# Optimization experiments

Hardware: AMD Instinct MI355X
Metric: run time of the kernel (lower is better)

## Reference

```python
import jax, jax.numpy as jnp
import numpy as np

N = 100000      # nodes
E = 1600000     # edges (avg degree 16)
F_IN = 300      # input feature dim
H = 64          # hidden channels
OUT = 20        # output classes
L = 8           # num GCN2Conv layers
ALPHA = 0.1
THETA = 0.5


def setup_inputs() -> dict:
    key = jax.random.key(0)
    ks = jax.random.split(key, 6)
    x = jax.random.normal(ks[0], (N, F_IN), jnp.float32)
    edge_index = jax.random.randint(ks[1], (2, E), 0, N, dtype=jnp.int32)
    edge_weights = jax.random.uniform(ks[2], (E,), jnp.float32)
    W_in = jax.random.normal(ks[3], (F_IN, H), jnp.float32) / np.sqrt(F_IN)
    b_in = jnp.zeros((H,), jnp.float32)
    conv_w = jax.random.normal(ks[4], (L, H, H), jnp.float32) / np.sqrt(H)
    W_out = jax.random.normal(ks[5], (H, OUT), jnp.float32) / np.sqrt(H)
    b_out = jnp.zeros((OUT,), jnp.float32)
    return dict(x=x, edge_index=edge_index, edge_weights=edge_weights,
                W_in=W_in, b_in=b_in, conv_w=conv_w, W_out=W_out, b_out=b_out)


def _gcn_norm(edge_index, edge_weights, n, dtype):
    # add self-loops with weight 1, symmetric normalization (PyG gcn_norm)
    loop = jnp.arange(n, dtype=edge_index.dtype)
    row = jnp.concatenate([edge_index[0], loop])
    col = jnp.concatenate([edge_index[1], loop])
    w = jnp.concatenate([edge_weights, jnp.ones((n,), dtype)])
    deg = jax.ops.segment_sum(w, col, num_segments=n)
    dinv = jnp.where(deg > 0, jax.lax.rsqrt(deg), 0.0).astype(dtype)
    norm = dinv[row] * w * dinv[col]
    return row, col, norm


def reference(x, edge_index, edge_weights, W_in, b_in, conv_w, W_out, b_out):
    n = x.shape[0]
    row, col, norm = _gcn_norm(edge_index, edge_weights, n, x.dtype)
    # eval mode: dropout is identity
    h = jax.nn.relu(x @ W_in + b_in)   # start_with_lin (F_IN != H)
    x0 = h
    num_layers = conv_w.shape[0]
    for l in range(num_layers):
        beta = float(np.log(THETA / (l + 1) + 1.0))
        # A_hat @ h : gather sources, weight by norm, scatter-add to targets
        agg = jax.ops.segment_sum(norm[:, None] * h[row], col, num_segments=n)
        z = (1.0 - ALPHA) * agg + ALPHA * x0  # initial-residual mixing
        h = jax.nn.relu((1.0 - beta) * z + beta * (z @ conv_w[l]))
    return h @ W_out + b_out
```

## Files before the change

### kernel.cpp

```cpp
#include <hip/hip_runtime.h>
#include <hip/hip_fp16.h>
#include <math.h>


#define HID 64
#define FIN 300
#define NOUT 20
#define ALPHA 0.1f
#define DSCALE 262144.0f
#define CNT_SHIFT 25
#define DEG_MASK 0x1FFFFFFu

typedef _Float16 f16;
typedef f16 f16x8 __attribute__((ext_vector_type(8)));
typedef float f32x4 __attribute__((ext_vector_type(4)));

__device__ __forceinline__ float wdec(unsigned v) {
    union { unsigned short u; __half h; } c;
    c.u = (unsigned short)(v >> 17);
    return __half2float(c.h);
}

__device__ __forceinline__ void unpack8(const float4& v, float* f) {
    const __half2* p = reinterpret_cast<const __half2*>(&v);
#pragma unroll
    for (int i = 0; i < 4; ++i) {
        float2 t = __half22float2(p[i]);
        f[2 * i] = t.x;
        f[2 * i + 1] = t.y;
    }
}

__global__ void init_k(unsigned* __restrict__ packed, int n) {
    int i = blockIdx.x * blockDim.x + threadIdx.x;
    if (i < n) packed[i] = 0u;
}

__global__ void accum_k(const int* __restrict__ col, const float* __restrict__ w,
                        unsigned* __restrict__ packed,
                        unsigned char* __restrict__ rank, int e) {
    int i = blockIdx.x * blockDim.x + threadIdx.x;
    if (i < e) {
        unsigned q = (unsigned)__float2uint_rn(w[i] * DSCALE);
        unsigned old = atomicAdd(&packed[col[i]], (1u << CNT_SHIFT) | q);
        rank[i] = (unsigned char)(old >> CNT_SHIFT);
    }
}

__global__ __launch_bounds__(1024) void unpackscan_k(const unsigned* __restrict__ packed,
                                                     float* __restrict__ dinv,
                                                     int* __restrict__ bsum, int n) {
    __shared__ int s[1024];
    int t = threadIdx.x, i = blockIdx.x * 1024 + t;
    int cnt = 0;
    if (i < n) {
        unsigned v = packed[i];
        cnt = (int)(v >> CNT_SHIFT);
        float d = 1.0f + (float)(v & DEG_MASK) * (1.0f / DSCALE);
        dinv[i] = rsqrtf(d);
    }
    s[t] = cnt;
    __syncthreads();
    for (int off = 512; off > 0; off >>= 1) {
        if (t < off) s[t] += s[t + off];
        __syncthreads();
    }
    if (t == 0) bsum[blockIdx.x] = s[0];
}

__global__ void scan2_k(int* __restrict__ bsum, int nb, int* __restrict__ rp,
                        int n, int e) {
    if (blockIdx.x == 0 && threadIdx.x == 0) {
        int acc = 0;
        for (int b = 0; b < nb; ++b) { int v = bsum[b]; bsum[b] = acc; acc += v; }
        rp[n] = e;
    }
}

__global__ __launch_bounds__(1024) void scan3_k(const unsigned* __restrict__ packed,
                                                const int* __restrict__ bsum,
                                                int* __restrict__ rp, int n) {
    __shared__ int s[1024];
    int t = threadIdx.x, i = blockIdx.x * 1024 + t;
    int v = (i < n) ? (int)(packed[i] >> CNT_SHIFT) : 0;
    s[t] = v;
    __syncthreads();
    for (int off = 1; off < 1024; off <<= 1) {
        int u = (t >= off) ? s[t - off] : 0;
        __syncthreads();
        s[t] += u;
        __syncthreads();
    }
    if (i < n) rp[i] = bsum[blockIdx.x] + s[t] - v;
}

__global__ __launch_bounds__(256) void fill_k(const int* __restrict__ row,
                                              const int* __restrict__ col,
                                              const float* __restrict__ ew,
                                              const float* __restrict__ dinv,
                                              const int* __restrict__ rp,
                                              const unsigned char* __restrict__ rank,
                                              unsigned* __restrict__ edges,
                                              int e, int n) {
    int xcd = blockIdx.x & 7;
    int lo = (int)(((long long)n * xcd) >> 3);
    int hi = (int)(((long long)n * (xcd + 1)) >> 3);
    int nblk = gridDim.x >> 3;
    int stride = nblk * 256;
    for (int i = (blockIdx.x >> 3) * 256 + threadIdx.x; i < e; i += stride) {
        int c = col[i];
        if (c < lo || c >= hi) continue;
        int r = row[i];
        float nw = (1.0f - ALPHA) * dinv[r] * ew[i] * dinv[c];
        union { __half h; unsigned short u; } cv;
        cv.h = __float2half(nw);
        int pos = rp[c] + (int)rank[i];
        edges[pos] = ((unsigned)cv.u << 17) | (unsigned)r;
    }
}

__global__ void wt_k(const float* __restrict__ Win, f16* __restrict__ Wt) {
    int i = blockIdx.x * blockDim.x + threadIdx.x;
    if (i < 64 * 320) {
        int c = i / 320, k = i - c * 320;
        Wt[i] = (k < FIN) ? (f16)Win[k * 64 + c] : (f16)0.0f;
    }
}

__global__ __launch_bounds__(256) void gemm_in_k(const float* __restrict__ x,
                                                 const f16* __restrict__ Wt,
                                                 const float* __restrict__ bin,
                                                 __half* __restrict__ x0h, int n) {
    __shared__ f16 As[64 * 72];
    int t = threadIdx.x, lane = t & 63, wv = t >> 6;
    int node0 = blockIdx.x * 64;
    int lr = lane & 15, kg = lane >> 4;
    f32x4 acc0 = {0, 0, 0, 0}, acc1 = {0, 0, 0, 0}, acc2 = {0, 0, 0, 0}, acc3 = {0, 0, 0, 0};
    int fi = t & 15;
    for (int c = 0; c < 5; ++c) {
        __syncthreads();
#pragma unroll
        for (int it = 0; it < 4; ++it) {
            int row = (t >> 4) + it * 16;
            int rr = node0 + row;
            rr = (rr < n) ? rr : (n - 1);
            int kbase = c * 64 + fi * 4;
            float4 v = make_float4(0.f, 0.f, 0.f, 0.f);
            if (kbase < FIN)
                v = *reinterpret_cast<const float4*>(x + (size_t)rr * FIN + kbase);
            union { float2 f2; f16 h[4]; } u;
            u.h[0] = (f16)v.x; u.h[1] = (f16)v.y; u.h[2] = (f16)v.z; u.h[3] = (f16)v.w;
            *reinterpret_cast<float2*>(As + row * 72 + fi * 4) = u.f2;
        }
        __syncthreads();
#pragma unroll
        for (int ks = 0; ks < 2; ++ks) {
            f16x8 a = *(const f16x8*)(As + (wv * 16 + lr) * 72 + ks * 32 + kg * 8);
            const f16* wb = Wt + c * 64 + ks * 32 + kg * 8;
            f16x8 b0 = *(const f16x8*)(wb + (0 * 16 + lr) * 320);
            f16x8 b1 = *(const f16x8*)(wb + (1 * 16 + lr) * 320);
            f16x8 b2 = *(const f16x8*)(wb + (2 * 16 + lr) * 320);
            f16x8 b3 = *(const f16x8*)(wb + (3 * 16 + lr) * 320);
            acc0 = __builtin_amdgcn_mfma_f32_16x16x32_f16(a, b0, acc0, 0, 0, 0);
            acc1 = __builtin_amdgcn_mfma_f32_16x16x32_f16(a, b1, acc1, 0, 0, 0);
            acc2 = __builtin_amdgcn_mfma_f32_16x16x32_f16(a, b2, acc2, 0, 0, 0);
            acc3 = __builtin_amdgcn_mfma_f32_16x16x32_f16(a, b3, acc3, 0, 0, 0);
        }
    }
    float bi0 = bin[0 * 16 + lr], bi1 = bin[1 * 16 + lr];
    float bi2 = bin[2 * 16 + lr], bi3 = bin[3 * 16 + lr];
    f16 ov[4][4];
#pragma unroll
    for (int r = 0; r < 4; ++r) {
        ov[0][r] = (f16)fmaxf(acc0[r] + bi0, 0.f);
        ov[1][r] = (f16)fmaxf(acc1[r] + bi1, 0.f);
        ov[2][r] = (f16)fmaxf(acc2[r] + bi2, 0.f);
        ov[3][r] = (f16)fmaxf(acc3[r] + bi3, 0.f);
    }
    __syncthreads();
#pragma unroll
    for (int cg = 0; cg < 4; ++cg)
#pragma unroll
        for (int r = 0; r < 4; ++r)
            As[(wv * 16 + kg * 4 + r) * 72 + cg * 16 + lr] = ov[cg][r];
    __syncthreads();
#pragma unroll
    for (int it = 0; it < 2; ++it) {
        int idx = t + it * 256;
        int row = idx >> 3, ch = idx & 7;
        int node = node0 + row;
        if (node < n)
            ((float4*)(x0h + (size_t)node * 64))[ch] =
                *reinterpret_cast<const float4*>(As + row * 72 + ch * 8);
    }
}

__global__ __launch_bounds__(256) void layer_k(const int* __restrict__ rp,
                                               const unsigned* __restrict__ edges,
                                               const float* __restrict__ dinv,
                                               const __half* __restrict__ x0h,
                                               const __half* __restrict__ hin,
                                               __half* __restrict__ hout,
                                               const float* __restrict__ Wl,
                                               float beta, int n) {
    __shared__ f16 As[64 * 72];
    __shared__ f16 Bs[64 * 72];
    int t = threadIdx.x, lane = t & 63, wv = t >> 6;
    int node0 = blockIdx.x * 64;
    for (int i = t; i < 4096; i += 256) {
        int k = i >> 6, c = i & 63;
        Bs[c * 72 + k] = (f16)Wl[i];
    }
    int g = lane >> 3, c8 = lane & 7;
#pragma unroll
    for (int pass = 0; pass < 2; ++pass) {
        int row = pass * 32 + wv * 8 + g;
        int node = node0 + row;
        int nd = (node < n) ? node : (n - 1);
        int j = rp[nd], end = (node < n) ? rp[nd + 1] : j;
        float a0[8], a1[8];
#pragma unroll
        for (int i = 0; i < 8; ++i) { a0[i] = 0.f; a1[i] = 0.f; }
        while (__any(j < end)) {
            bool v0 = j < end, v1 = (j + 1) < end;
            unsigned e0 = edges[v0 ? j : 0];
            unsigned e1 = edges[v1 ? (j + 1) : 0];
            float w0 = v0 ? wdec(e0) : 0.f;
            float w1 = v1 ? wdec(e1) : 0.f;
            float4 r0 = ((const float4*)(hin + (size_t)(e0 & 0x1FFFF) * 64))[c8];
            float4 r1 = ((const float4*)(hin + (size_t)(e1 & 0x1FFFF) * 64))[c8];
            float f0[8], f1[8];
            unpack8(r0, f0);
            unpack8(r1, f1);
#pragma unroll
            for (int i = 0; i < 8; ++i) {
                a0[i] = fmaf(w0, f0[i], a0[i]);
                a1[i] = fmaf(w1, f1[i], a1[i]);
            }
            j += 2;
        }
        float di = dinv[nd];
        float c1 = (1.0f - ALPHA) * di * di;
        float4 hs4 = ((const float4*)(hin + (size_t)nd * 64))[c8];
        float4 xs4 = ((const float4*)(x0h + (size_t)nd * 64))[c8];
        float hf[8], xf[8];
        unpack8(hs4, hf);
        unpack8(xs4, xf);
        f16x8 zv8;
#pragma unroll
        for (int i = 0; i < 8; ++i)
            zv8[i] = (f16)fmaf(ALPHA, xf[i], fmaf(c1, hf[i], a0[i] + a1[i]));
        *(f16x8*)(As + row * 72 + c8 * 8) = zv8;
    }
    __syncthreads();
    int lr = lane & 15, kg = lane >> 4;
    f32x4 acc0 = {0, 0, 0, 0}, acc1 = {0, 0, 0, 0}, acc2 = {0, 0, 0, 0}, acc3 = {0, 0, 0, 0};
    f16x8 af0 = *(const f16x8*)(As + (wv * 16 + lr) * 72 + kg * 8);
    f16x8 af1 = *(const f16x8*)(As + (wv * 16 + lr) * 72 + 32 + kg * 8);
    {
        f16x8 b0 = *(const f16x8*)(Bs + (0 * 16 + lr) * 72 + kg * 8);
        f16x8 b1 = *(const f16x8*)(Bs + (0 * 16 + lr) * 72 + 32 + kg * 8);
        acc0 = __builtin_amdgcn_mfma_f32_16x16x32_f16(af0, b0, acc0, 0, 0, 0);
        acc0 = __builtin_amdgcn_mfma_f32_16x16x32_f16(af1, b1, acc0, 0, 0, 0);
    }
    {
        f16x8 b0 = *(const f16x8*)(Bs + (1 * 16 + lr) * 72 + kg * 8);
        f16x8 b1 = *(const f16x8*)(Bs + (1 * 16 + lr) * 72 + 32 + kg * 8);
        acc1 = __builtin_amdgcn_mfma_f32_16x16x32_f16(af0, b0, acc1, 0, 0, 0);
        acc1 = __builtin_amdgcn_mfma_f32_16x16x32_f16(af1, b1, acc1, 0, 0, 0);
    }
    {
        f16x8 b0 = *(const f16x8*)(Bs + (2 * 16 + lr) * 72 + kg * 8);
        f16x8 b1 = *(const f16x8*)(Bs + (2 * 16 + lr) * 72 + 32 + kg * 8);
        acc2 = __builtin_amdgcn_mfma_f32_16x16x32_f16(af0, b0, acc2, 0, 0, 0);
        acc2 = __builtin_amdgcn_mfma_f32_16x16x32_f16(af1, b1, acc2, 0, 0, 0);
    }
    {
        f16x8 b0 = *(const f16x8*)(Bs + (3 * 16 + lr) * 72 + kg * 8);
        f16x8 b1 = *(const f16x8*)(Bs + (3 * 16 + lr) * 72 + 32 + kg * 8);
        acc3 = __builtin_amdgcn_mfma_f32_16x16x32_f16(af0, b0, acc3, 0, 0, 0);
        acc3 = __builtin_amdgcn_mfma_f32_16x16x32_f16(af1, b1, acc3, 0, 0, 0);
    }
    float omb = 1.0f - beta;
    f16 ov[4][4];
#pragma unroll
    for (int cg = 0; cg < 4; ++cg) {
        f32x4 acc = (cg == 0) ? acc0 : (cg == 1) ? acc1 : (cg == 2) ? acc2 : acc3;
        int col = cg * 16 + lr;
#pragma unroll
        for (int r = 0; r < 4; ++r) {
            float zv = (float)As[(wv * 16 + kg * 4 + r) * 72 + col];
            ov[cg][r] = (f16)fmaxf(fmaf(beta, acc[r], omb * zv), 0.f);
        }
    }
    __syncthreads();
#pragma unroll
    for (int cg = 0; cg < 4; ++cg)
#pragma unroll
        for (int r = 0; r < 4; ++r)
            As[(wv * 16 + kg * 4 + r) * 72 + cg * 16 + lr] = ov[cg][r];
    __syncthreads();
#pragma unroll
    for (int it = 0; it < 2; ++it) {
        int idx = t + it * 256;
        int row = idx >> 3, ch = idx & 7;
        int node = node0 + row;
        if (node < n)
            ((float4*)(hout + (size_t)node * 64))[ch] =
                *reinterpret_cast<const float4*>(As + row * 72 + ch * 8);
    }
}

__global__ __launch_bounds__(256) void gemm_out_k(const __half* __restrict__ h,
                                                  const float* __restrict__ Wout,
                                                  const float* __restrict__ bout,
                                                  float* __restrict__ out, int n) {
    __shared__ float hs[64][65];
    __shared__ float Ws[64 * NOUT];
    __shared__ float bs[NOUT];
    int t = threadIdx.x;
    for (int i = t; i < 64 * NOUT; i += 256) Ws[i] = Wout[i];
    if (t < NOUT) bs[t] = bout[t];
    int base = blockIdx.x * 64;
    int lim = min(64, n - base);
    for (int i = t; i < 64 * 32; i += 256) {
        int r = i >> 5, c2 = (i & 31) * 2;
        float2 v = make_float2(0.f, 0.f);
        if (r < lim) {
            __half2 hv = reinterpret_cast<const __half2*>(
                h + (size_t)(base + r) * 64)[i & 31];
            v = __half22float2(hv);
        }
        hs[r][c2] = v.x;
        hs[r][c2 + 1] = v.y;
    }
    __syncthreads();
#pragma unroll
    for (int q = 0; q < 5; ++q) {
        int of = t + 256 * q;
        int nd = of / NOUT, o = of - nd * NOUT;
        float acc = bs[o];
#pragma unroll
        for (int k = 0; k < 64; ++k) acc = fmaf(hs[nd][k], Ws[k * NOUT + o], acc);
        if (nd < lim) out[(size_t)(base + nd) * NOUT + o] = acc;
    }
}

extern "C" void kernel_launch(void* const* d_in, const int* in_sizes, int n_in,
                              void* d_out, int out_size, void* d_ws, size_t ws_size,
                              hipStream_t stream) {
    const float* x    = (const float*)d_in[0];
    const int*   ei   = (const int*)d_in[1];
    const float* ew   = (const float*)d_in[2];
    const float* Win  = (const float*)d_in[3];
    const float* bin  = (const float*)d_in[4];
    const float* cw   = (const float*)d_in[5];
    const float* Wout = (const float*)d_in[6];
    const float* bout = (const float*)d_in[7];

    const int n = in_sizes[0] / FIN;
    const int e = in_sizes[2];
    const int L = in_sizes[5] / (HID * HID);
    const int* row = ei;
    const int* col = ei + e;

    size_t off = 0;
    auto alloc = [&](size_t bytes) -> char* {
        char* q = (char*)d_ws + off;
        off = (off + bytes + 255) & ~(size_t)255;
        return q;
    };
    __half* x0h  = (__half*)alloc((size_t)n * HID * 2);
    __half* hA   = (__half*)alloc((size_t)n * HID * 2);
    __half* hB   = (__half*)alloc((size_t)n * HID * 2);
    unsigned* edges = (unsigned*)alloc((size_t)e * 4);
    unsigned char* rank = (unsigned char*)alloc((size_t)e);
    unsigned* packed = (unsigned*)alloc((size_t)n * 4);
    float* dinv  = (float*)alloc((size_t)n * 4);
    int*   rp    = (int*)alloc((size_t)(n + 1) * 4);
    int*   bsum  = (int*)alloc(1024 * 4);
    f16*   Wt    = (f16*)alloc((size_t)64 * 320 * 2);

    const int nb = (n + 1023) / 1024;
    const int ntile = (n + 63) / 64;

    init_k<<<(n + 255) / 256, 256, 0, stream>>>(packed, n);
    accum_k<<<(e + 255) / 256, 256, 0, stream>>>(col, ew, packed, rank, e);
    unpackscan_k<<<nb, 1024, 0, stream>>>(packed, dinv, bsum, n);
    scan2_k<<<1, 1, 0, stream>>>(bsum, nb, rp, n, e);
    scan3_k<<<nb, 1024, 0, stream>>>(packed, bsum, rp, n);
    fill_k<<<1024, 256, 0, stream>>>(row, col, ew, dinv, rp, rank, edges, e, n);

    wt_k<<<(64 * 320 + 255) / 256, 256, 0, stream>>>(Win, Wt);
    gemm_in_k<<<ntile, 256, 0, stream>>>(x, Wt, bin, x0h, n);

    const __half* hin = x0h;
    __half* hout = hA;
    for (int l = 0; l < L; ++l) {
        float beta = (float)log(0.5 / (double)(l + 1) + 1.0);
        layer_k<<<ntile, 256, 0, stream>>>(rp, edges, dinv, x0h, hin, hout,
                                           cw + (size_t)l * HID * HID, beta, n);
        hin = hout;
        hout = (hout == hA) ? hB : hA;
    }
    gemm_out_k<<<(n + 63) / 64, 256, 0, stream>>>(hin, Wout, bout, (float*)d_out, n);
}
```

Measured before the change: 498.6 us.

## Pad CSR rows to multiples of four and privatize degree atomics across eight copies

The CSR build now splits the degree/count atomics across eight privatized copies selected by block index, which cuts atomic contention. It records per-copy offsets so edges can still be placed. Each node's edge list is padded to a multiple of four with zeroed entries, so the aggregation loop can load four edges at once with a single uint4 read and keep four independent accumulators. The cost is more setup memory traffic (8x packed array, zeroing the padded edge buffer, extra offset tables), plus up to three padded zero-weight gathers of node 0 per row in every layer.

```diff
diff --git a/kernel.cpp b/kernel.cpp
--- a/kernel.cpp
+++ b/kernel.cpp
@@ -31,35 +31,49 @@
     }
 }
 
-__global__ void init_k(unsigned* __restrict__ packed, int n) {
+__global__ void zero_k(unsigned* __restrict__ p, int nwords) {
     int i = blockIdx.x * blockDim.x + threadIdx.x;
-    if (i < n) packed[i] = 0u;
+    if (i < nwords) p[i] = 0u;
 }
 
 __global__ void accum_k(const int* __restrict__ col, const float* __restrict__ w,
-                        unsigned* __restrict__ packed,
-                        unsigned char* __restrict__ rank, int e) {
+                        unsigned* __restrict__ packed8,
+                        unsigned short* __restrict__ rank16, int e, int n) {
     int i = blockIdx.x * blockDim.x + threadIdx.x;
     if (i < e) {
+        int copy = blockIdx.x & 7;
         unsigned q = (unsigned)__float2uint_rn(w[i] * DSCALE);
-        unsigned old = atomicAdd(&packed[col[i]], (1u << CNT_SHIFT) | q);
-        rank[i] = (unsigned char)(old >> CNT_SHIFT);
-    }
-}
-
-__global__ __launch_bounds__(1024) void unpackscan_k(const unsigned* __restrict__ packed,
+        unsigned old = atomicAdd(&packed8[(size_t)copy * n + col[i]],
+                                 (1u << CNT_SHIFT) | q);
+        rank16[i] = (unsigned short)(((old >> CNT_SHIFT) & 0xFFu) | (copy << 8));
+    }
+}
+
+__global__ __launch_bounds__(1024) void unpackscan_k(const unsigned* __restrict__ packed8,
                                                      float* __restrict__ dinv,
+                                                     unsigned char* __restrict__ off8,
+                                                     int* __restrict__ padcnt,
                                                      int* __restrict__ bsum, int n) {
     __shared__ int s[1024];
     int t = threadIdx.x, i = blockIdx.x * 1024 + t;
-    int cnt = 0;
+    int pad = 0;
     if (i < n) {
-        unsigned v = packed[i];
-        cnt = (int)(v >> CNT_SHIFT);
-        float d = 1.0f + (float)(v & DEG_MASK) * (1.0f / DSCALE);
+        unsigned cnt = 0, dsum = 0;
+        union { unsigned char b[8]; uint2 u2; } offs;
+#pragma unroll
+        for (int k = 0; k < 8; ++k) {
+            unsigned v = packed8[(size_t)k * n + i];
+            offs.b[k] = (unsigned char)cnt;
+            cnt += (v >> CNT_SHIFT);
+            dsum += (v & DEG_MASK);
+        }
+        float d = 1.0f + (float)dsum * (1.0f / DSCALE);
         dinv[i] = rsqrtf(d);
-    }
-    s[t] = cnt;
+        reinterpret_cast<uint2*>(off8)[i] = offs.u2;
+        pad = (int)((cnt + 3u) & ~3u);
+        padcnt[i] = pad;
+    }
+    s[t] = pad;
     __syncthreads();
     for (int off = 512; off > 0; off >>= 1) {
         if (t < off) s[t] += s[t + off];
@@ -68,21 +82,20 @@
     if (t == 0) bsum[blockIdx.x] = s[0];
 }
 
-__global__ void scan2_k(int* __restrict__ bsum, int nb, int* __restrict__ rp,
-                        int n, int e) {
+__global__ void scan2_k(int* __restrict__ bsum, int nb, int* __restrict__ rp, int n) {
     if (blockIdx.x == 0 && threadIdx.x == 0) {
         int acc = 0;
         for (int b = 0; b < nb; ++b) { int v = bsum[b]; bsum[b] = acc; acc += v; }
-        rp[n] = e;
-    }
-}
-
-__global__ __launch_bounds__(1024) void scan3_k(const unsigned* __restrict__ packed,
+        rp[n] = acc;
+    }
+}
+
+__global__ __launch_bounds__(1024) void scan3_k(const int* __restrict__ padcnt,
                                                 const int* __restrict__ bsum,
                                                 int* __restrict__ rp, int n) {
     __shared__ int s[1024];
     int t = threadIdx.x, i = blockIdx.x * 1024 + t;
-    int v = (i < n) ? (int)(packed[i] >> CNT_SHIFT) : 0;
+    int v = (i < n) ? padcnt[i] : 0;
     s[t] = v;
     __syncthreads();
     for (int off = 1; off < 1024; off <<= 1) {
@@ -99,7 +112,8 @@
                                               const float* __restrict__ ew,
                                               const float* __restrict__ dinv,
                                               const int* __restrict__ rp,
-                                              const unsigned char* __restrict__ rank,
+                                              const unsigned short* __restrict__ rank16,
+                                              const unsigned char* __restrict__ off8,
                                               unsigned* __restrict__ edges,
                                               int e, int n) {
     int xcd = blockIdx.x & 7;
@@ -114,7 +128,8 @@
         float nw = (1.0f - ALPHA) * dinv[r] * ew[i] * dinv[c];
         union { __half h; unsigned short u; } cv;
         cv.h = __float2half(nw);
-        int pos = rp[c] + (int)rank[i];
+        unsigned short rk = rank16[i];
+        int pos = rp[c] + (int)off8[c * 8 + (rk >> 8)] + (int)(rk & 0xFFu);
         edges[pos] = ((unsigned)cv.u << 17) | (unsigned)r;
     }
 }
@@ -218,26 +233,33 @@
         int node = node0 + row;
         int nd = (node < n) ? node : (n - 1);
         int j = rp[nd], end = (node < n) ? rp[nd + 1] : j;
-        float a0[8], a1[8];
-#pragma unroll
-        for (int i = 0; i < 8; ++i) { a0[i] = 0.f; a1[i] = 0.f; }
+        float a0[8], a1[8], a2[8], a3[8];
+#pragma unroll
+        for (int i = 0; i < 8; ++i) { a0[i] = 0.f; a1[i] = 0.f; a2[i] = 0.f; a3[i] = 0.f; }
         while (__any(j < end)) {
-            bool v0 = j < end, v1 = (j + 1) < end;
-            unsigned e0 = edges[v0 ? j : 0];
-            unsigned e1 = edges[v1 ? (j + 1) : 0];
-            float w0 = v0 ? wdec(e0) : 0.f;
-            float w1 = v1 ? wdec(e1) : 0.f;
-            float4 r0 = ((const float4*)(hin + (size_t)(e0 & 0x1FFFF) * 64))[c8];
-            float4 r1 = ((const float4*)(hin + (size_t)(e1 & 0x1FFFF) * 64))[c8];
-            float f0[8], f1[8];
+            bool v = j < end;
+            uint4 e4 = *reinterpret_cast<const uint4*>(edges + (v ? j : 0));
+            float w0 = v ? wdec(e4.x) : 0.f;
+            float w1 = v ? wdec(e4.y) : 0.f;
+            float w2 = v ? wdec(e4.z) : 0.f;
+            float w3 = v ? wdec(e4.w) : 0.f;
+            float4 r0 = ((const float4*)(hin + (size_t)(e4.x & 0x1FFFF) * 64))[c8];
+            float4 r1 = ((const float4*)(hin + (size_t)(e4.y & 0x1FFFF) * 64))[c8];
+            float4 r2 = ((const float4*)(hin + (size_t)(e4.z & 0x1FFFF) * 64))[c8];
+            float4 r3 = ((const float4*)(hin + (size_t)(e4.w & 0x1FFFF) * 64))[c8];
+            float f0[8], f1[8], f2[8], f3[8];
             unpack8(r0, f0);
             unpack8(r1, f1);
+            unpack8(r2, f2);
+            unpack8(r3, f3);
 #pragma unroll
             for (int i = 0; i < 8; ++i) {
                 a0[i] = fmaf(w0, f0[i], a0[i]);
                 a1[i] = fmaf(w1, f1[i], a1[i]);
+                a2[i] = fmaf(w2, f2[i], a2[i]);
+                a3[i] = fmaf(w3, f3[i], a3[i]);
             }
-            j += 2;
+            j += 4;
         }
         float di = dinv[nd];
         float c1 = (1.0f - ALPHA) * di * di;
@@ -249,7 +271,8 @@
         f16x8 zv8;
 #pragma unroll
         for (int i = 0; i < 8; ++i)
-            zv8[i] = (f16)fmaf(ALPHA, xf[i], fmaf(c1, hf[i], a0[i] + a1[i]));
+            zv8[i] = (f16)fmaf(ALPHA, xf[i],
+                               fmaf(c1, hf[i], (a0[i] + a1[i]) + (a2[i] + a3[i])));
         *(f16x8*)(As + row * 72 + c8 * 8) = zv8;
     }
     __syncthreads();
@@ -363,6 +386,7 @@
     const int L = in_sizes[5] / (HID * HID);
     const int* row = ei;
     const int* col = ei + e;
+    const int epadmax = e + 3 * n + 64;
 
     size_t off = 0;
     auto alloc = [&](size_t bytes) -> char* {
@@ -373,10 +397,12 @@
     __half* x0h  = (__half*)alloc((size_t)n * HID * 2);
     __half* hA   = (__half*)alloc((size_t)n * HID * 2);
     __half* hB   = (__half*)alloc((size_t)n * HID * 2);
-    unsigned* edges = (unsigned*)alloc((size_t)e * 4);
-    unsigned char* rank = (unsigned char*)alloc((size_t)e);
-    unsigned* packed = (unsigned*)alloc((size_t)n * 4);
+    unsigned* edges = (unsigned*)alloc((size_t)epadmax * 4);
+    unsigned short* rank16 = (unsigned short*)alloc((size_t)e * 2);
+    unsigned* packed8 = (unsigned*)alloc((size_t)8 * n * 4);
+    unsigned char* off8 = (unsigned char*)alloc((size_t)n * 8);
     float* dinv  = (float*)alloc((size_t)n * 4);
+    int*   padcnt= (int*)alloc((size_t)n * 4);
     int*   rp    = (int*)alloc((size_t)(n + 1) * 4);
     int*   bsum  = (int*)alloc(1024 * 4);
     f16*   Wt    = (f16*)alloc((size_t)64 * 320 * 2);
@@ -384,12 +410,13 @@
     const int nb = (n + 1023) / 1024;
     const int ntile = (n + 63) / 64;
 
-    init_k<<<(n + 255) / 256, 256, 0, stream>>>(packed, n);
-    accum_k<<<(e + 255) / 256, 256, 0, stream>>>(col, ew, packed, rank, e);
-    unpackscan_k<<<nb, 1024, 0, stream>>>(packed, dinv, bsum, n);
-    scan2_k<<<1, 1, 0, stream>>>(bsum, nb, rp, n, e);
-    scan3_k<<<nb, 1024, 0, stream>>>(packed, bsum, rp, n);
-    fill_k<<<1024, 256, 0, stream>>>(row, col, ew, dinv, rp, rank, edges, e, n);
+    zero_k<<<(8 * n + 255) / 256, 256, 0, stream>>>(packed8, 8 * n);
+    zero_k<<<(epadmax + 255) / 256, 256, 0, stream>>>(edges, epadmax);
+    accum_k<<<(e + 255) / 256, 256, 0, stream>>>(col, ew, packed8, rank16, e, n);
+    unpackscan_k<<<nb, 1024, 0, stream>>>(packed8, dinv, off8, padcnt, bsum, n);
+    scan2_k<<<1, 1, 0, stream>>>(bsum, nb, rp, n);
+    scan3_k<<<nb, 1024, 0, stream>>>(padcnt, bsum, rp, n);
+    fill_k<<<1024, 256, 0, stream>>>(row, col, ew, dinv, rp, rank16, off8, edges, e, n);
 
     wt_k<<<(64 * 320 + 255) / 256, 256, 0, stream>>>(Win, Wt);
     gemm_in_k<<<ntile, 256, 0, stream>>>(x, Wt, bin, x0h, n);
```

Result: slower. 523.5 us (+5.0%).
